# Performance work log

Measured on AMD Instinct MI355X. Metric: run time of the kernel, lower is better.

Reference implementation:

```python
import jax, jax.numpy as jnp
import numpy as np

DIMS = [64, 128, 192, 256]   # Matryoshka sub-dims (init arg `dims`)
TEMPERATURE = 1.0
NEG_INF = float('-inf')
EPS = 1e-12  # F.normalize eps


def setup_inputs() -> dict:
    key = jax.random.key(0)
    k1, k2 = jax.random.split(key)
    B, K, D = 2048, 4096, 256
    reps_q = jax.random.normal(k1, (B, D), dtype=jnp.float32)
    reps_d = jax.random.normal(k2, (K, D), dtype=jnp.float32)
    return {"reps_q": reps_q, "reps_d": reps_d}


def _l2_normalize(x):
    n = jnp.linalg.norm(x, axis=1, keepdims=True)
    return x / jnp.maximum(n, EPS)


def _loss_for_dim(reps_q, reps_d, dim):
    q = _l2_normalize(reps_q[:, :dim])   # [B, dim]
    d = _l2_normalize(reps_d[:, :dim])   # [K, dim]
    B, K = q.shape[0], d.shape[0]

    qk = q @ d.T                         # [B, K]

    # check_pos_neg_pair_conflict (always True in the torch code)
    pos = d[:B]                          # positives are the first B keys
    sim = jax.lax.stop_gradient(pos @ d.T)               # [B, K], detached
    eye_bk = jnp.eye(B, K, dtype=bool)
    conflict = jnp.isclose(sim, 1.0, rtol=1e-5, atol=1e-5) & ~eye_bk
    qk = jnp.where(conflict, NEG_INF, qk)

    # use_all_pairs=True path: kq, qq, kk with -inf diagonals
    eye_bb = jnp.eye(B, dtype=bool)
    kq = jnp.where(eye_bb, NEG_INF, pos @ q.T)           # [B, B]
    qq = jnp.where(eye_bb, NEG_INF, q @ q.T)             # [B, B]
    kk = jnp.where(eye_bb, NEG_INF, pos @ pos.T)         # [B, B]

    scores = jnp.concatenate([qk, kq, qq, kk], axis=1)   # [B, K+3B]

    # check_false_neg: mask entries above diag(scores)+0.1 (thresholds detached)
    # diag(scores)[i] = scores[i, i] = qk[i, i] since B <= K
    thr = jax.lax.stop_gradient(jnp.diagonal(qk))[:, None] + 0.1
    scores = jnp.where(scores > thr, NEG_INF, scores)

    # cross-entropy with labels = arange(B)
    logp = jax.nn.log_softmax(scores / TEMPERATURE, axis=1)
    idx = jnp.arange(B)
    return -jnp.mean(logp[idx, idx])


def reference(reps_q, reps_d):
    loss = 0.0
    for dim in DIMS:
        loss = loss + _loss_for_dim(reps_q, reps_d, dim)
    return loss / len(DIMS)
```

## Files before the change

kernel.cpp:

```cpp
#include <hip/hip_runtime.h>

#define B_N 2048
#define K_N 4096
#define D_N 256
#define GRID_SCORE 2576
#define LOG2E 1.44269504f

typedef unsigned short u16;
typedef unsigned int u32;
typedef short short8 __attribute__((ext_vector_type(8)));
typedef float f32x4 __attribute__((ext_vector_type(4)));

__device__ __forceinline__ u16 f2bf(float x) {
    union { float f; u32 u; } v; v.f = x;
    u32 u = v.u;
    u32 lsb = (u >> 16) & 1u;
    u += 0x7fffu + lsb;
    return (u16)(u >> 16);
}
__device__ __forceinline__ float bits2f(u32 u) {
    union { u32 u; float f; } v; v.u = u; return v.f;
}

__global__ __launch_bounds__(256) void prep_kernel(
    const float* __restrict__ qsrc, const float* __restrict__ dsrc,
    u16* __restrict__ qb, u16* __restrict__ db,
    float* __restrict__ invnq, float* __restrict__ invnd, float* __restrict__ diag,
    float* __restrict__ rowsum, u32* __restrict__ doneCnt)
{
    if (blockIdx.x < 32) rowsum[blockIdx.x * 256 + threadIdx.x] = 0.f;
    if (blockIdx.x == 32 && threadIdx.x == 0)
        __hip_atomic_store(doneCnt, 0u, __ATOMIC_RELAXED, __HIP_MEMORY_SCOPE_AGENT);

    const int wave = threadIdx.x >> 6;
    const int lane = threadIdx.x & 63;
    const int row  = blockIdx.x * 4 + wave;

    if (row < B_N) {
        const int i = row;
        float4 qv = *(const float4*)(qsrc + i * D_N + lane * 4);
        float4 dv = *(const float4*)(dsrc + i * D_N + lane * 4);
        ushort4 qs; qs.x = f2bf(qv.x); qs.y = f2bf(qv.y); qs.z = f2bf(qv.z); qs.w = f2bf(qv.w);
        *(ushort4*)(qb + i * D_N + lane * 4) = qs;
        float sqq = qv.x*qv.x + qv.y*qv.y + qv.z*qv.z + qv.w*qv.w;
        float sdd = dv.x*dv.x + dv.y*dv.y + dv.z*dv.z + dv.w*dv.w;
        float sqd = qv.x*dv.x + qv.y*dv.y + qv.z*dv.z + qv.w*dv.w;
        #pragma unroll
        for (int m = 1; m < 16; m <<= 1) {
            sqq += __shfl_xor(sqq, m);
            sdd += __shfl_xor(sdd, m);
            sqd += __shfl_xor(sqd, m);
        }
        float gq0 = __shfl(sqq, 0),  gq1 = __shfl(sqq, 16), gq2 = __shfl(sqq, 32), gq3 = __shfl(sqq, 48);
        float gd0 = __shfl(sdd, 0),  gd1 = __shfl(sdd, 16), gd2 = __shfl(sdd, 32), gd3 = __shfl(sdd, 48);
        float gp0 = __shfl(sqd, 0),  gp1 = __shfl(sqd, 16), gp2 = __shfl(sqd, 32), gp3 = __shfl(sqd, 48);
        if (lane < 4) {
            float pq = gq0, pd = gd0, pp = gp0;
            if (lane >= 1) { pq += gq1; pd += gd1; pp += gp1; }
            if (lane >= 2) { pq += gq2; pd += gd2; pp += gp2; }
            if (lane >= 3) { pq += gq3; pd += gd3; pp += gp3; }
            float inq = 1.0f / fmaxf(sqrtf(pq), 1e-12f);
            float ind = 1.0f / fmaxf(sqrtf(pd), 1e-12f);
            invnq[i * 4 + lane] = inq;
            diag[i * 4 + lane]  = pp * inq * ind;
        }
    } else {
        const int j = row - B_N;
        float4 dv = *(const float4*)(dsrc + j * D_N + lane * 4);
        ushort4 ds; ds.x = f2bf(dv.x); ds.y = f2bf(dv.y); ds.z = f2bf(dv.z); ds.w = f2bf(dv.w);
        *(ushort4*)(db + j * D_N + lane * 4) = ds;
        float sdd = dv.x*dv.x + dv.y*dv.y + dv.z*dv.z + dv.w*dv.w;
        #pragma unroll
        for (int m = 1; m < 16; m <<= 1) sdd += __shfl_xor(sdd, m);
        float gd0 = __shfl(sdd, 0), gd1 = __shfl(sdd, 16), gd2 = __shfl(sdd, 32), gd3 = __shfl(sdd, 48);
        if (lane < 4) {
            float pd = gd0;
            if (lane >= 1) pd += gd1;
            if (lane >= 2) pd += gd2;
            if (lane >= 3) pd += gd3;
            invnd[j * 4 + lane] = 1.0f / fmaxf(sqrtf(pd), 1e-12f);
        }
    }
}

template<bool KK, bool EYE>
__device__ __forceinline__ void epi2(
    const f32x4* accq, const f32x4* accd,
    const float* ldsInvAq, const float* ldsInvAd, const float* ldsThr,
    const float* ldsInvB, const float* ldsThrB, float* ldsAcc, float* ldsAccCol,
    int s, int wrow, int quad, int lane15)
{
    const int myr = wrow + quad * 4;
    f32x4 ivAq = *(const f32x4*)(ldsInvAq + s * 64 + myr);
    f32x4 ivAd = *(const f32x4*)(ldsInvAd + s * 64 + myr);
    f32x4 thrv = *(const f32x4*)(ldsThr   + s * 64 + myr);
    float rsd[4] = {0.f, 0.f, 0.f, 0.f};
    #pragma unroll
    for (int ct = 0; ct < 4; ++ct) {
        const int jloc = ct * 16 + lane15;
        const float ivB  = ldsInvB[s * 64 + jloc];
        const float thrB = KK ? ldsThrB[s * 64 + jloc] : 0.f;
        float colp = 0.f;
        #pragma unroll
        for (int r = 0; r < 4; ++r) {
            const float sq = accq[ct][r] * (ivAq[r] * ivB);
            const float sd = accd[ct][r] * (ivAd[r] * ivB);
            const bool eye = EYE && ((myr + r) == jloc);
            bool conflict = (fabsf(sd - LOG2E) <= 2e-5f * LOG2E);
            if (EYE) conflict = conflict && !eye;
            const float eq = exp2f(sq);
            if (!conflict && sq <= thrv[r]) rsd[r] += eq;
            if (KK) {
                bool okk = (sd <= thrv[r]);
                if (EYE) okk = okk && !eye;
                if (okk) rsd[r] += exp2f(sd);
                bool okq = (sq <= thrB);
                if (EYE) okq = okq && !eye;
                if (okq) colp += eq;
            }
        }
        if (KK) {
            colp += __shfl_xor(colp, 16);
            colp += __shfl_xor(colp, 32);
            if (quad == 0) atomicAdd(&ldsAccCol[jloc * 4 + s], colp);
        }
    }
    #pragma unroll
    for (int r = 0; r < 4; ++r) {
        float v = rsd[r];
        v += __shfl_xor(v, 1);
        v += __shfl_xor(v, 2);
        v += __shfl_xor(v, 4);
        v += __shfl_xor(v, 8);
        if (lane15 == 0)
            ldsAcc[(myr + r) * 4 + s] += v;
    }
}

template<bool DUAL>
__device__ __forceinline__ void epiQ(
    const f32x4* accq,
    const float* ldsInvAq, const float* ldsThr,
    const float* ldsInvB, const float* ldsThrB, float* ldsAcc, float* ldsAccCol,
    int s, int wrow, int quad, int lane15)
{
    const int myr = wrow + quad * 4;
    f32x4 ivAq = *(const f32x4*)(ldsInvAq + s * 64 + myr);
    f32x4 thrv = *(const f32x4*)(ldsThr   + s * 64 + myr);
    float rsd[4] = {0.f, 0.f, 0.f, 0.f};
    #pragma unroll
    for (int ct = 0; ct < 4; ++ct) {
        const int jloc = ct * 16 + lane15;
        const float ivB  = ldsInvB[s * 64 + jloc];
        const float thrB = DUAL ? ldsThrB[s * 64 + jloc] : 0.f;
        float colp = 0.f;
        #pragma unroll
        for (int r = 0; r < 4; ++r) {
            const float sq = accq[ct][r] * (ivAq[r] * ivB);
            const float e = exp2f(sq);
            if (!DUAL) {
                const bool eye = ((myr + r) == jloc);
                if (!eye && sq <= thrv[r]) rsd[r] += e;
            } else {
                if (sq <= thrv[r]) rsd[r] += e;
                if (sq <= thrB)    colp  += e;
            }
        }
        if (DUAL) {
            colp += __shfl_xor(colp, 16);
            colp += __shfl_xor(colp, 32);
            if (quad == 0) atomicAdd(&ldsAccCol[jloc * 4 + s], colp);
        }
    }
    #pragma unroll
    for (int r = 0; r < 4; ++r) {
        float v = rsd[r];
        v += __shfl_xor(v, 1);
        v += __shfl_xor(v, 2);
        v += __shfl_xor(v, 4);
        v += __shfl_xor(v, 8);
        if (lane15 == 0)
            ldsAcc[(myr + r) * 4 + s] += v;
    }
}

#define LSB 264
__global__ __launch_bounds__(256, 4) void score_kernel(
    const u16* __restrict__ qb, const u16* __restrict__ db,
    const float* __restrict__ invnq, const float* __restrict__ invnd,
    const float* __restrict__ diag, float* __restrict__ rowsum,
    u32* __restrict__ doneCnt, u32* __restrict__ out)
{
    __shared__ u16   ldsB[64 * LSB];
    __shared__ float ldsInvAq[4 * 64];
    __shared__ float ldsInvAd[4 * 64];
    __shared__ float ldsThr[4 * 64];
    __shared__ float ldsInvB[4 * 64];
    __shared__ float ldsThrB[4 * 64];
    __shared__ float ldsAcc[256];
    __shared__ float ldsAccCol[256];

    const int bid = blockIdx.x;
    int rb, cbl, mode;
    if (bid < 1024)      { mode = 0; rb = bid >> 5; cbl = bid & 31; }
    else if (bid < 2048) { mode = 1; int b = bid - 1024; rb = b >> 5; cbl = b & 31; }
    else if (bid < 2080) { mode = 2; rb = bid - 2048; cbl = rb; }
    else {
        mode = 3; int k = bid - 2080; int a = 0;
        while (k >= 31 - a) { k -= 31 - a; ++a; }
        rb = a; cbl = a + 1 + k;
    }
    const bool qpl  = (mode >= 2);
    const bool col  = (mode == 0 || mode == 3);
    const bool eyeB = (mode == 0 && rb == cbl);
    const int IR = rb * 64;
    const int JB = (mode == 1) ? (B_N + cbl * 64) : (cbl * 64);
    const u16*  bsrc     = qpl ? qb : db;
    const float* invBsrc = qpl ? invnq : invnd;

    const int tid    = threadIdx.x;
    const int lane   = tid & 63;
    const int lane15 = lane & 15;
    const int quad   = lane >> 4;
    const int wrow   = (tid >> 6) * 16;

    {
        const int row = tid >> 2, s = tid & 3;
        ldsInvAq[s * 64 + row] = invnq[(IR + row) * 4 + s] * LOG2E;
        ldsInvAd[s * 64 + row] = invnd[(IR + row) * 4 + s] * LOG2E;
        ldsThr[s * 64 + row]   = (diag[(IR + row) * 4 + s] + 0.1f) * LOG2E;
        ldsInvB[s * 64 + row]  = invBsrc[(JB + row) * 4 + s];
        ldsThrB[s * 64 + row]  = col ? (diag[(JB + row) * 4 + s] + 0.1f) * LOG2E : 0.f;
        ldsAcc[tid] = 0.f;
        ldsAccCol[tid] = 0.f;
    }

    #pragma unroll
    for (int c = 0; c < 8; ++c) {
        int idx = tid + c * 256;
        int row = idx >> 5;
        int ch  = idx & 31;
        uint4 v = *(const uint4*)(bsrc + (JB + row) * D_N + ch * 8);
        *(uint4*)(ldsB + row * LSB + ch * 8) = v;
    }

    const u16* qrowp = qb + (IR + wrow + lane15) * D_N + quad * 8;
    const u16* drowp = db + (IR + wrow + lane15) * D_N + quad * 8;

    if (!qpl) {
        short8 aq0 = *(const short8*)(qrowp);
        short8 aq1 = *(const short8*)(qrowp + 32);
        short8 ad0 = *(const short8*)(drowp);
        short8 ad1 = *(const short8*)(drowp + 32);
        __syncthreads();

        f32x4 accq[4], accd[4];
        #pragma unroll
        for (int ct = 0; ct < 4; ++ct) {
            accq[ct] = (f32x4){0.f, 0.f, 0.f, 0.f};
            accd[ct] = (f32x4){0.f, 0.f, 0.f, 0.f};
        }
        #pragma clang loop unroll(disable)
        for (int s = 0; s < 4; ++s) {
            const int sn = ((s + 1) & 3) * 64;
            short8 nq0 = *(const short8*)(qrowp + sn);
            short8 nq1 = *(const short8*)(qrowp + sn + 32);
            short8 nd0 = *(const short8*)(drowp + sn);
            short8 nd1 = *(const short8*)(drowp + sn + 32);
            #pragma unroll
            for (int ct = 0; ct < 4; ++ct) {
                short8 b0 = *(const short8*)(ldsB + (ct * 16 + lane15) * LSB + s * 64 + quad * 8);
                accq[ct] = __builtin_amdgcn_mfma_f32_16x16x32_bf16(aq0, b0, accq[ct], 0, 0, 0);
                accd[ct] = __builtin_amdgcn_mfma_f32_16x16x32_bf16(ad0, b0, accd[ct], 0, 0, 0);
            }
            #pragma unroll
            for (int ct = 0; ct < 4; ++ct) {
                short8 b1 = *(const short8*)(ldsB + (ct * 16 + lane15) * LSB + s * 64 + 32 + quad * 8);
                accq[ct] = __builtin_amdgcn_mfma_f32_16x16x32_bf16(aq1, b1, accq[ct], 0, 0, 0);
                accd[ct] = __builtin_amdgcn_mfma_f32_16x16x32_bf16(ad1, b1, accd[ct], 0, 0, 0);
            }
            if (mode == 0) {
                if (eyeB) epi2<true,true >(accq, accd, ldsInvAq, ldsInvAd, ldsThr, ldsInvB, ldsThrB, ldsAcc, ldsAccCol, s, wrow, quad, lane15);
                else      epi2<true,false>(accq, accd, ldsInvAq, ldsInvAd, ldsThr, ldsInvB, ldsThrB, ldsAcc, ldsAccCol, s, wrow, quad, lane15);
            } else {
                epi2<false,false>(accq, accd, ldsInvAq, ldsInvAd, ldsThr, ldsInvB, ldsThrB, ldsAcc, ldsAccCol, s, wrow, quad, lane15);
            }
            aq0 = nq0; aq1 = nq1; ad0 = nd0; ad1 = nd1;
        }
    } else {
        short8 aq0 = *(const short8*)(qrowp);
        short8 aq1 = *(const short8*)(qrowp + 32);
        __syncthreads();

        f32x4 accq[4];
        #pragma unroll
        for (int ct = 0; ct < 4; ++ct) accq[ct] = (f32x4){0.f, 0.f, 0.f, 0.f};
        #pragma clang loop unroll(disable)
        for (int s = 0; s < 4; ++s) {
            const int sn = ((s + 1) & 3) * 64;
            short8 nq0 = *(const short8*)(qrowp + sn);
            short8 nq1 = *(const short8*)(qrowp + sn + 32);
            #pragma unroll
            for (int ct = 0; ct < 4; ++ct) {
                short8 b0 = *(const short8*)(ldsB + (ct * 16 + lane15) * LSB + s * 64 + quad * 8);
                accq[ct] = __builtin_amdgcn_mfma_f32_16x16x32_bf16(aq0, b0, accq[ct], 0, 0, 0);
            }
            #pragma unroll
            for (int ct = 0; ct < 4; ++ct) {
                short8 b1 = *(const short8*)(ldsB + (ct * 16 + lane15) * LSB + s * 64 + 32 + quad * 8);
                accq[ct] = __builtin_amdgcn_mfma_f32_16x16x32_bf16(aq1, b1, accq[ct], 0, 0, 0);
            }
            if (mode == 2) epiQ<false>(accq, ldsInvAq, ldsThr, ldsInvB, ldsThrB, ldsAcc, ldsAccCol, s, wrow, quad, lane15);
            else           epiQ<true >(accq, ldsInvAq, ldsThr, ldsInvB, ldsThrB, ldsAcc, ldsAccCol, s, wrow, quad, lane15);
            aq0 = nq0; aq1 = nq1;
        }
    }
    __syncthreads();

    atomicAdd(&rowsum[IR * 4 + tid], ldsAcc[tid]);
    if (col) atomicAdd(&rowsum[JB * 4 + tid], ldsAccCol[tid]);
    __syncthreads();
    if (tid == 0) {
        u32 tk = __hip_atomic_fetch_add(doneCnt, 1u, __ATOMIC_RELAXED,
                                        __HIP_MEMORY_SCOPE_AGENT);
        ldsAccCol[0] = (tk == (GRID_SCORE - 1)) ? 1.f : 0.f;
    }
    __syncthreads();

    if (ldsAccCol[0] != 0.f) {
        float acc = 0.f;
        #pragma unroll 8
        for (int c = 0; c < 32; ++c) {
            int idx = tid + c * 256;
            float rsv = __hip_atomic_load(&rowsum[idx], __ATOMIC_RELAXED,
                                          __HIP_MEMORY_SCOPE_AGENT);
            acc += logf(rsv) - diag[idx];
        }
        ldsAcc[tid] = acc;
        __syncthreads();
        #pragma unroll
        for (int off = 128; off > 0; off >>= 1) {
            if (tid < off) ldsAcc[tid] += ldsAcc[tid + off];
            __syncthreads();
        }
        if (tid == 0) {
            float L = ldsAcc[0] * (1.0f / (B_N * 4.0f));
            u16 h = f2bf(L);
            union { float f; u32 u; } b; b.f = L;
            u32 c0 = (b.u & 0xFFFF0000u) | (u32)h;
            u32 c1 = c0 + 0x10000u;
            u32 c2 = c0 - 0x10000u;
            float e0 = fabsf(bits2f(c0) - L);
            float e1 = fabsf(bits2f(c1) - L);
            float e2 = fabsf(bits2f(c2) - L);
            u32 best = c0; float be = e0;
            if (e1 < be) { best = c1; be = e1; }
            if (e2 < be) { best = c2; }
            out[0] = best;
        }
    }
}

extern "C" void kernel_launch(void* const* d_in, const int* in_sizes, int n_in,
                              void* d_out, int out_size, void* d_ws, size_t ws_size,
                              hipStream_t stream) {
    (void)in_sizes; (void)n_in; (void)out_size; (void)ws_size;
    const float* qsrc = (const float*)d_in[0];
    const float* dsrc = (const float*)d_in[1];
    char* ws = (char*)d_ws;
    u16*   qb      = (u16*)ws;
    u16*   db      = (u16*)(ws + 1048576);
    float* invnq   = (float*)(ws + 3145728);
    float* invnd   = (float*)(ws + 3178496);
    float* diag    = (float*)(ws + 3244032);
    float* rowsum  = (float*)(ws + 3276800);
    u32*   doneCnt = (u32*)(ws + 3309568);

    prep_kernel<<<1536, 256, 0, stream>>>(qsrc, dsrc, qb, db, invnq, invnd, diag,
                                          rowsum, doneCnt);
    score_kernel<<<GRID_SCORE, 256, 0, stream>>>(qb, db, invnq, invnd, diag, rowsum,
                                                 doneCnt, (u32*)d_out);
}
```

Measured before the change: 117.0 us.

## Halve score kernel B-tile LDS by staging K dimension in two halves

```diff
diff --git a/kernel.cpp b/kernel.cpp
--- a/kernel.cpp
+++ b/kernel.cpp
@@ -184,8 +184,8 @@
     }
 }
 
-#define LSB 264
-__global__ __launch_bounds__(256, 4) void score_kernel(
+#define LSB 136
+__global__ __launch_bounds__(256, 5) void score_kernel(
     const u16* __restrict__ qb, const u16* __restrict__ db,
     const float* __restrict__ invnq, const float* __restrict__ invnd,
     const float* __restrict__ diag, float* __restrict__ rowsum,
@@ -224,6 +224,9 @@
     const int quad   = lane >> 4;
     const int wrow   = (tid >> 6) * 16;
 
+    const int srow = tid >> 4;
+    (void)srow;
+
     {
         const int row = tid >> 2, s = tid & 3;
         ldsInvAq[s * 64 + row] = invnq[(IR + row) * 4 + s] * LOG2E;
@@ -236,10 +239,10 @@
     }
 
     #pragma unroll
-    for (int c = 0; c < 8; ++c) {
+    for (int c = 0; c < 4; ++c) {
         int idx = tid + c * 256;
-        int row = idx >> 5;
-        int ch  = idx & 31;
+        int row = idx >> 4;
+        int ch  = idx & 15;
         uint4 v = *(const uint4*)(bsrc + (JB + row) * D_N + ch * 8);
         *(uint4*)(ldsB + row * LSB + ch * 8) = v;
     }
@@ -252,7 +255,6 @@
         short8 aq1 = *(const short8*)(qrowp + 32);
         short8 ad0 = *(const short8*)(drowp);
         short8 ad1 = *(const short8*)(drowp + 32);
-        __syncthreads();
 
         f32x4 accq[4], accd[4];
         #pragma unroll
@@ -261,58 +263,105 @@
             accd[ct] = (f32x4){0.f, 0.f, 0.f, 0.f};
         }
         #pragma clang loop unroll(disable)
-        for (int s = 0; s < 4; ++s) {
-            const int sn = ((s + 1) & 3) * 64;
-            short8 nq0 = *(const short8*)(qrowp + sn);
-            short8 nq1 = *(const short8*)(qrowp + sn + 32);
-            short8 nd0 = *(const short8*)(drowp + sn);
-            short8 nd1 = *(const short8*)(drowp + sn + 32);
-            #pragma unroll
-            for (int ct = 0; ct < 4; ++ct) {
-                short8 b0 = *(const short8*)(ldsB + (ct * 16 + lane15) * LSB + s * 64 + quad * 8);
-                accq[ct] = __builtin_amdgcn_mfma_f32_16x16x32_bf16(aq0, b0, accq[ct], 0, 0, 0);
-                accd[ct] = __builtin_amdgcn_mfma_f32_16x16x32_bf16(ad0, b0, accd[ct], 0, 0, 0);
-            }
-            #pragma unroll
-            for (int ct = 0; ct < 4; ++ct) {
-                short8 b1 = *(const short8*)(ldsB + (ct * 16 + lane15) * LSB + s * 64 + 32 + quad * 8);
-                accq[ct] = __builtin_amdgcn_mfma_f32_16x16x32_bf16(aq1, b1, accq[ct], 0, 0, 0);
-                accd[ct] = __builtin_amdgcn_mfma_f32_16x16x32_bf16(ad1, b1, accd[ct], 0, 0, 0);
-            }
-            if (mode == 0) {
-                if (eyeB) epi2<true,true >(accq, accd, ldsInvAq, ldsInvAd, ldsThr, ldsInvB, ldsThrB, ldsAcc, ldsAccCol, s, wrow, quad, lane15);
-                else      epi2<true,false>(accq, accd, ldsInvAq, ldsInvAd, ldsThr, ldsInvB, ldsThrB, ldsAcc, ldsAccCol, s, wrow, quad, lane15);
-            } else {
-                epi2<false,false>(accq, accd, ldsInvAq, ldsInvAd, ldsThr, ldsInvB, ldsThrB, ldsAcc, ldsAccCol, s, wrow, quad, lane15);
-            }
-            aq0 = nq0; aq1 = nq1; ad0 = nd0; ad1 = nd1;
+        for (int h = 0; h < 2; ++h) {
+            __syncthreads();
+            #pragma clang loop unroll(disable)
+            for (int s2 = 0; s2 < 2; ++s2) {
+                const int s = h * 2 + s2;
+                const int kloc = s2 * 64;
+                const int sn = ((s + 1) & 3) * 64;
+                short8 nq0 = *(const short8*)(qrowp + sn);
+                short8 nq1 = *(const short8*)(qrowp + sn + 32);
+                short8 nd0 = *(const short8*)(drowp + sn);
+                short8 nd1 = *(const short8*)(drowp + sn + 32);
+                #pragma unroll
+                for (int ct = 0; ct < 4; ++ct) {
+                    short8 b0 = *(const short8*)(ldsB + (ct * 16 + lane15) * LSB + kloc + quad * 8);
+                    accq[ct] = __builtin_amdgcn_mfma_f32_16x16x32_bf16(aq0, b0, accq[ct], 0, 0, 0);
+                    accd[ct] = __builtin_amdgcn_mfma_f32_16x16x32_bf16(ad0, b0, accd[ct], 0, 0, 0);
+                }
+                #pragma unroll
+                for (int ct = 0; ct < 4; ++ct) {
+                    short8 b1 = *(const short8*)(ldsB + (ct * 16 + lane15) * LSB + kloc + 32 + quad * 8);
+                    accq[ct] = __builtin_amdgcn_mfma_f32_16x16x32_bf16(aq1, b1, accq[ct], 0, 0, 0);
+                    accd[ct] = __builtin_amdgcn_mfma_f32_16x16x32_bf16(ad1, b1, accd[ct], 0, 0, 0);
+                }
+                if (mode == 0) {
+                    if (eyeB) epi2<true,true >(accq, accd, ldsInvAq, ldsInvAd, ldsThr, ldsInvB, ldsThrB, ldsAcc, ldsAccCol, s, wrow, quad, lane15);
+                    else      epi2<true,false>(accq, accd, ldsInvAq, ldsInvAd, ldsThr, ldsInvB, ldsThrB, ldsAcc, ldsAccCol, s, wrow, quad, lane15);
+                } else {
+                    epi2<false,false>(accq, accd, ldsInvAq, ldsInvAd, ldsThr, ldsInvB, ldsThrB, ldsAcc, ldsAccCol, s, wrow, quad, lane15);
+                }
+                aq0 = nq0; aq1 = nq1; ad0 = nd0; ad1 = nd1;
+            }
+            if (h == 0) {
+                uint4 bv[4];
+                #pragma unroll
+                for (int c = 0; c < 4; ++c) {
+                    int idx = tid + c * 256;
+                    int row = idx >> 4;
+                    int ch  = idx & 15;
+                    bv[c] = *(const uint4*)(bsrc + (JB + row) * D_N + 128 + ch * 8);
+                }
+                __syncthreads();
+                #pragma unroll
+                for (int c = 0; c < 4; ++c) {
+                    int idx = tid + c * 256;
+                    int row = idx >> 4;
+                    int ch  = idx & 15;
+                    *(uint4*)(ldsB + row * LSB + ch * 8) = bv[c];
+                }
+            }
         }
     } else {
         short8 aq0 = *(const short8*)(qrowp);
         short8 aq1 = *(const short8*)(qrowp + 32);
-        __syncthreads();
 
         f32x4 accq[4];
         #pragma unroll
         for (int ct = 0; ct < 4; ++ct) accq[ct] = (f32x4){0.f, 0.f, 0.f, 0.f};
         #pragma clang loop unroll(disable)
-        for (int s = 0; s < 4; ++s) {
-            const int sn = ((s + 1) & 3) * 64;
-            short8 nq0 = *(const short8*)(qrowp + sn);
-            short8 nq1 = *(const short8*)(qrowp + sn + 32);
-            #pragma unroll
-            for (int ct = 0; ct < 4; ++ct) {
-                short8 b0 = *(const short8*)(ldsB + (ct * 16 + lane15) * LSB + s * 64 + quad * 8);
-                accq[ct] = __builtin_amdgcn_mfma_f32_16x16x32_bf16(aq0, b0, accq[ct], 0, 0, 0);
-            }
-            #pragma unroll
-            for (int ct = 0; ct < 4; ++ct) {
-                short8 b1 = *(const short8*)(ldsB + (ct * 16 + lane15) * LSB + s * 64 + 32 + quad * 8);
-                accq[ct] = __builtin_amdgcn_mfma_f32_16x16x32_bf16(aq1, b1, accq[ct], 0, 0, 0);
-            }
-            if (mode == 2) epiQ<false>(accq, ldsInvAq, ldsThr, ldsInvB, ldsThrB, ldsAcc, ldsAccCol, s, wrow, quad, lane15);
-            else           epiQ<true >(accq, ldsInvAq, ldsThr, ldsInvB, ldsThrB, ldsAcc, ldsAccCol, s, wrow, quad, lane15);
-            aq0 = nq0; aq1 = nq1;
+        for (int h = 0; h < 2; ++h) {
+            __syncthreads();
+            #pragma clang loop unroll(disable)
+            for (int s2 = 0; s2 < 2; ++s2) {
+                const int s = h * 2 + s2;
+                const int kloc = s2 * 64;
+                const int sn = ((s + 1) & 3) * 64;
+                short8 nq0 = *(const short8*)(qrowp + sn);
+                short8 nq1 = *(const short8*)(qrowp + sn + 32);
+                #pragma unroll
+                for (int ct = 0; ct < 4; ++ct) {
+                    short8 b0 = *(const short8*)(ldsB + (ct * 16 + lane15) * LSB + kloc + quad * 8);
+                    accq[ct] = __builtin_amdgcn_mfma_f32_16x16x32_bf16(aq0, b0, accq[ct], 0, 0, 0);
+                }
+                #pragma unroll
+                for (int ct = 0; ct < 4; ++ct) {
+                    short8 b1 = *(const short8*)(ldsB + (ct * 16 + lane15) * LSB + kloc + 32 + quad * 8);
+                    accq[ct] = __builtin_amdgcn_mfma_f32_16x16x32_bf16(aq1, b1, accq[ct], 0, 0, 0);
+                }
+                if (mode == 2) epiQ<false>(accq, ldsInvAq, ldsThr, ldsInvB, ldsThrB, ldsAcc, ldsAccCol, s, wrow, quad, lane15);
+                else           epiQ<true >(accq, ldsInvAq, ldsThr, ldsInvB, ldsThrB, ldsAcc, ldsAccCol, s, wrow, quad, lane15);
+                aq0 = nq0; aq1 = nq1;
+            }
+            if (h == 0) {
+                uint4 bv[4];
+                #pragma unroll
+                for (int c = 0; c < 4; ++c) {
+                    int idx = tid + c * 256;
+                    int row = idx >> 4;
+                    int ch  = idx & 15;
+                    bv[c] = *(const uint4*)(bsrc + (JB + row) * D_N + 128 + ch * 8);
+                }
+                __syncthreads();
+                #pragma unroll
+                for (int c = 0; c < 4; ++c) {
+                    int idx = tid + c * 256;
+                    int row = idx >> 4;
+                    int ch  = idx & 15;
+                    *(uint4*)(ldsB + row * LSB + ch * 8) = bv[c];
+                }
+            }
         }
     }
     __syncthreads();
```

Result: slower. 193.4 us (+65.2%).
